# Performance work log

Hardware: AMD Instinct MI355X
Metric: run time of the kernel (lower is better)

## Reference

```python
import jax, jax.numpy as jnp
import numpy as np

NUM_FIELDS = 39
VOCAB_PER_FIELD = 1000
EMB = 64
HEADS = 2
LAYERS = 3
BATCH = 16384
FLAT = NUM_FIELDS * EMB  # 2496


def _mhsa(x, Wq, Wk, Wv, Wr):
    # x: [B, n, D]; no scaling (scaling=False in source)
    B, n, D = x.shape
    dh = D // HEADS
    q = (x @ Wq).reshape(B, n, HEADS, dh)
    k = (x @ Wk).reshape(B, n, HEADS, dh)
    v = (x @ Wv).reshape(B, n, HEADS, dh)
    scores = jnp.einsum('bihd,bjhd->bhij', q, k)
    attn = jax.nn.softmax(scores, axis=-1)
    out = jnp.einsum('bhij,bjhd->bihd', attn, v).reshape(B, n, D)
    out = out + x @ Wr  # residual projection (use_res=True)
    return jax.nn.relu(out)


def setup_inputs() -> dict:
    key = jax.random.key(0)
    ks = jax.random.split(key, 12)
    X = jax.random.randint(ks[0], (BATCH, NUM_FIELDS), 0, VOCAB_PER_FIELD, dtype=jnp.int64 if jax.config.jax_enable_x64 else jnp.int32)
    emb_table = jax.random.normal(ks[1], (NUM_FIELDS * VOCAB_PER_FIELD, EMB), jnp.float32) * 0.05
    WQ = jax.random.normal(ks[2], (LAYERS, EMB, EMB), jnp.float32) * 0.05
    WK = jax.random.normal(ks[3], (LAYERS, EMB, EMB), jnp.float32) * 0.05
    WV = jax.random.normal(ks[4], (LAYERS, EMB, EMB), jnp.float32) * 0.05
    WR = jax.random.normal(ks[5], (LAYERS, EMB, EMB), jnp.float32) * 0.05
    W1 = jax.random.normal(ks[6], (FLAT, 512), jnp.float32) * 0.02
    b1 = jnp.zeros((512,), jnp.float32)
    W2 = jax.random.normal(ks[7], (512, 256), jnp.float32) * 0.02
    b2 = jnp.zeros((256,), jnp.float32)
    W3 = jax.random.normal(ks[8], (256, 1), jnp.float32) * 0.02
    b3 = jnp.zeros((1,), jnp.float32)
    Wlin = jax.random.normal(ks[9], (FLAT, 1), jnp.float32) * 0.02
    return {"X": X, "emb_table": emb_table, "WQ": WQ, "WK": WK, "WV": WV,
            "WR": WR, "W1": W1, "b1": b1, "W2": W2, "b2": b2, "W3": W3,
            "b3": b3, "Wlin": Wlin}


def reference(X, emb_table, WQ, WK, WV, WR, W1, b1, W2, b2, W3, b3, Wlin):
    offsets = jnp.arange(NUM_FIELDS, dtype=X.dtype) * VOCAB_PER_FIELD
    embed_x = emb_table[X + offsets[None, :]]  # [B, n, D]
    att = embed_x
    for i in range(LAYERS):
        att = _mhsa(att, WQ[i], WK[i], WV[i], WR[i])
    B = att.shape[0]
    att_output = jax.nn.relu(att.reshape(B, FLAT) @ Wlin)  # [B,1]
    # MLP: relu follows every Dense, including final 1-unit layer; dropout inactive
    h = embed_x.reshape(B, FLAT)
    h = jax.nn.relu(h @ W1 + b1)
    h = jax.nn.relu(h @ W2 + b2)
    dnn_output = jax.nn.relu(h @ W3 + b3)  # [B,1]
    return jax.nn.sigmoid(att_output + dnn_output)
```

## Files before the change

### kernel.cpp

```cpp
#include <hip/hip_runtime.h>
#include <hip/hip_bf16.h>


#define NF     39
#define EMB    64
#define NLAYER 3
#define VOCAB  1000
#define FLAT   2496
#define H1     512
#define H2     256

typedef __attribute__((ext_vector_type(8))) short  short8;
typedef __attribute__((ext_vector_type(4))) float  floatx4;

__device__ __forceinline__ short8 ld8s(const unsigned short* p) {
    return *(const short8*)p;
}
__device__ __forceinline__ float b2f(unsigned short h) {
    union { unsigned u; float f; } x; x.u = ((unsigned)h) << 16; return x.f;
}
__device__ __forceinline__ unsigned short f2b(float f) {
    union { float f; unsigned u; } x; x.f = f;
    unsigned u = x.u;
    return (unsigned short)((u + 0x7fffu + ((u >> 16) & 1u)) >> 16);
}
__device__ __forceinline__ unsigned cvt_pk(float a, float b) {
#if defined(__gfx950__)
    unsigned r;
    asm("v_cvt_pk_bf16_f32 %0, %1, %2" : "=v"(r) : "v"(a), "v"(b));
    return r;
#else
    return (unsigned)f2b(a) | ((unsigned)f2b(b) << 16);
#endif
}

__global__ void attw_t(const float* __restrict__ WQ, const float* __restrict__ WK,
                       const float* __restrict__ WV, const float* __restrict__ WR,
                       unsigned short* __restrict__ wqt, unsigned short* __restrict__ wkt,
                       unsigned short* __restrict__ wvt, unsigned short* __restrict__ wrt)
{
    int idx = blockIdx.x * 256 + threadIdx.x;
    if (idx >= 4 * 3 * 4096) return;
    int mat = idx / 12288;
    int rem = idx % 12288;
    int l   = rem / 4096;
    int ok  = rem % 4096;
    int o = ok >> 6, k = ok & 63;
    const float*    src = (mat == 0) ? WQ : (mat == 1) ? WK : (mat == 2) ? WV : WR;
    unsigned short* dst = (mat == 0) ? wqt : (mat == 1) ? wkt : (mat == 2) ? wvt : wrt;
    dst[l * 4096 + o * 64 + k] = f2b(src[l * 4096 + k * 64 + o]);
}

__global__ void w1pack(const float* __restrict__ W1, unsigned short* __restrict__ w1p)
{
    int t = blockIdx.x * 256 + threadIdx.x;
    int lane = t & 63, grp = t >> 6;
    int ot = grp / 78, kk = grp % 78;
    int q = lane >> 4, n = ot * 16 + (lane & 15);
    int kb = kk * 32 + q * 8;
    unsigned short* dst = w1p + grp * 512 + lane * 8;
    #pragma unroll
    for (int j = 0; j < 8; ++j)
        dst[j] = f2b(W1[(kb + j) * 512 + n]);
}

__global__ void w2pack(const float* __restrict__ W2, unsigned short* __restrict__ w2p)
{
    int t = blockIdx.x * 256 + threadIdx.x;
    int lane = t & 63, grp = t >> 6;
    int ot = grp / 16, kk = grp % 16;
    int q = lane >> 4, n = ot * 16 + (lane & 15);
    int kb = kk * 32 + q * 8;
    unsigned short* dst = w2p + grp * 512 + lane * 8;
    #pragma unroll
    for (int j = 0; j < 8; ++j)
        dst[j] = f2b(W2[(kb + j) * 256 + n]);
}

__global__ void __launch_bounds__(256) attn_kernel(
    const int* __restrict__ X,
    const float* __restrict__ embf,
    const unsigned short* __restrict__ wqt,
    const unsigned short* __restrict__ wkt,
    const unsigned short* __restrict__ wvt,
    const unsigned short* __restrict__ wrt,
    const float* __restrict__ wlinf,
    float* __restrict__ att_out)
{
    __shared__ unsigned short xs[2][48 * 72];
    __shared__ unsigned short arena[4][4736];
    __shared__ float red[4];

    const int tid  = threadIdx.x;
    const int wid  = tid >> 6;
    const int lane = tid & 63;
    const int sl   = wid >> 1;
    const int h    = wid & 1;
    const int quad = lane >> 4;
    const int l16  = lane & 15;
    const int samp = blockIdx.x * 2 + sl;

    unsigned short* xss = xs[sl];
    unsigned short* qs  = arena[wid];
    unsigned short* ks  = qs + 1920;
    unsigned short* Ps  = qs;
    unsigned short* vt  = qs + 3456;

    {
        const int tq = lane >> 4;
        const int cp = (lane & 15) * 2;
        const int col = h * 32 + cp;
        const int* xrow = X + samp * NF;
        #pragma unroll
        for (int t0 = 0; t0 < 48; t0 += 4) {
            int t = t0 + tq;
            unsigned pk = 0;
            if (t < NF) {
                int row = xrow[t] + t * VOCAB;
                const float2 v = *(const float2*)&embf[row * EMB + col];
                pk = cvt_pk(v.x, v.y);
            }
            *(unsigned*)&xss[t * 72 + col] = pk;
        }
    }
    __syncthreads();

    for (int layer = 0; layer < NLAYER; ++layer) {
        const unsigned short* wq  = wqt + layer * 4096;
        const unsigned short* wk  = wkt + layer * 4096;
        const unsigned short* wvp = wvt + layer * 4096;
        const unsigned short* wr  = wrt + layer * 4096;

        #pragma unroll
        for (int mat = 0; mat < 2; ++mat) {
            const unsigned short* wt = mat ? wk : wq;
            unsigned short* dst = mat ? ks : qs;
            #pragma unroll
            for (int mt = 0; mt < 3; ++mt) {
                #pragma unroll
                for (int nt = 0; nt < 2; ++nt) {
                    floatx4 c = {0.f, 0.f, 0.f, 0.f};
                    #pragma unroll
                    for (int kk = 0; kk < 2; ++kk) {
                        short8 a = ld8s(&xss[(mt * 16 + l16) * 72 + kk * 32 + quad * 8]);
                        short8 b = ld8s(&wt[(h * 32 + nt * 16 + l16) * 64 + kk * 32 + quad * 8]);
                        c = __builtin_amdgcn_mfma_f32_16x16x32_bf16(a, b, c, 0, 0, 0);
                    }
                    unsigned plo = cvt_pk(c[0], c[1]);
                    unsigned phi = cvt_pk(c[2], c[3]);
                    int base = (mt * 16 + quad * 4) * 40 + nt * 16 + l16;
                    dst[base]       = (unsigned short)plo;
                    dst[base + 40]  = (unsigned short)(plo >> 16);
                    dst[base + 80]  = (unsigned short)phi;
                    dst[base + 120] = (unsigned short)(phi >> 16);
                }
            }
        }

        floatx4 ST[3][3];
        #pragma unroll
        for (int jt = 0; jt < 3; ++jt) {
            short8 a = ld8s(&ks[(jt * 16 + l16) * 40 + quad * 8]);
            #pragma unroll
            for (int it = 0; it < 3; ++it) {
                short8 b = ld8s(&qs[(it * 16 + l16) * 40 + quad * 8]);
                floatx4 z = {0.f, 0.f, 0.f, 0.f};
                ST[jt][it] = __builtin_amdgcn_mfma_f32_16x16x32_bf16(a, b, z, 0, 0, 0);
            }
        }

        #pragma unroll
        for (int it = 0; it < 3; ++it) {
            float p[3][4];
            float sum = 0.f;
            #pragma unroll
            for (int jt = 0; jt < 3; ++jt)
                #pragma unroll
                for (int r = 0; r < 4; ++r) {
                    int j = jt * 16 + quad * 4 + r;
                    float e = (j < NF) ? __expf(ST[jt][it][r]) : 0.f;
                    p[jt][r] = e;
                    sum += e;
                }
            sum += __shfl_xor(sum, 16, 64);
            sum += __shfl_xor(sum, 32, 64);
            float inv = 1.0f / sum;
            #pragma unroll
            for (int jt = 0; jt < 3; ++jt) {
                uint2 w;
                w.x = cvt_pk(p[jt][0] * inv, p[jt][1] * inv);
                w.y = cvt_pk(p[jt][2] * inv, p[jt][3] * inv);
                *(uint2*)&Ps[(it * 16 + l16) * 72 + jt * 16 + quad * 4] = w;
            }
            uint2 z2; z2.x = 0; z2.y = 0;
            *(uint2*)&Ps[(it * 16 + l16) * 72 + 48 + quad * 4] = z2;
        }

        unsigned sv[2][2];
        #pragma unroll
        for (int mt = 0; mt < 3; ++mt) {
            #pragma unroll
            for (int nt = 0; nt < 2; ++nt) {
                floatx4 c = {0.f, 0.f, 0.f, 0.f};
                #pragma unroll
                for (int kk = 0; kk < 2; ++kk) {
                    short8 a = ld8s(&xss[(mt * 16 + l16) * 72 + kk * 32 + quad * 8]);
                    short8 b = ld8s(&wvp[(h * 32 + nt * 16 + l16) * 64 + kk * 32 + quad * 8]);
                    c = __builtin_amdgcn_mfma_f32_16x16x32_bf16(a, b, c, 0, 0, 0);
                }
                unsigned lo = cvt_pk(c[0], c[1]);
                unsigned hi = cvt_pk(c[2], c[3]);
                if (mt < 2) {
                    uint2 w; w.x = lo; w.y = hi;
                    *(uint2*)&vt[(nt * 16 + l16) * 40 + mt * 16 + quad * 4] = w;
                } else {
                    sv[nt][0] = lo; sv[nt][1] = hi;
                }
            }
        }

        floatx4 O[3][2];
        #pragma unroll
        for (int mt = 0; mt < 3; ++mt) {
            #pragma unroll
            for (int nt = 0; nt < 2; ++nt) {
                floatx4 c = {0.f, 0.f, 0.f, 0.f};
                #pragma unroll
                for (int kk = 0; kk < 2; ++kk) {
                    short8 a = ld8s(&xss[(mt * 16 + l16) * 72 + kk * 32 + quad * 8]);
                    short8 b = ld8s(&wr[(h * 32 + nt * 16 + l16) * 64 + kk * 32 + quad * 8]);
                    c = __builtin_amdgcn_mfma_f32_16x16x32_bf16(a, b, c, 0, 0, 0);
                }
                O[mt][nt] = c;
            }
        }

        __syncthreads();

        {
            short8 a0 = ld8s(&Ps[(l16) * 72 + quad * 8]);
            short8 a1 = ld8s(&Ps[(16 + l16) * 72 + quad * 8]);
            short8 a2 = ld8s(&Ps[(32 + l16) * 72 + quad * 8]);
            #pragma unroll
            for (int nt = 0; nt < 2; ++nt) {
                short8 b = ld8s(&vt[(nt * 16 + l16) * 40 + quad * 8]);
                O[0][nt] = __builtin_amdgcn_mfma_f32_16x16x32_bf16(a0, b, O[0][nt], 0, 0, 0);
                O[1][nt] = __builtin_amdgcn_mfma_f32_16x16x32_bf16(a1, b, O[1][nt], 0, 0, 0);
                O[2][nt] = __builtin_amdgcn_mfma_f32_16x16x32_bf16(a2, b, O[2][nt], 0, 0, 0);
            }
        }
        #pragma unroll
        for (int nt = 0; nt < 2; ++nt) {
            uint2 w; w.x = sv[nt][0]; w.y = sv[nt][1];
            *(uint2*)&vt[(nt * 16 + l16) * 40 + quad * 4] = w;
            uint2 z; z.x = 0; z.y = 0;
            *(uint2*)&vt[(nt * 16 + l16) * 40 + 16 + quad * 4] = z;
        }
        {
            short8 a0 = ld8s(&Ps[(l16) * 72 + 32 + quad * 8]);
            short8 a1 = ld8s(&Ps[(16 + l16) * 72 + 32 + quad * 8]);
            short8 a2 = ld8s(&Ps[(32 + l16) * 72 + 32 + quad * 8]);
            #pragma unroll
            for (int nt = 0; nt < 2; ++nt) {
                short8 b = ld8s(&vt[(nt * 16 + l16) * 40 + quad * 8]);
                O[0][nt] = __builtin_amdgcn_mfma_f32_16x16x32_bf16(a0, b, O[0][nt], 0, 0, 0);
                O[1][nt] = __builtin_amdgcn_mfma_f32_16x16x32_bf16(a1, b, O[1][nt], 0, 0, 0);
                O[2][nt] = __builtin_amdgcn_mfma_f32_16x16x32_bf16(a2, b, O[2][nt], 0, 0, 0);
            }
        }

        #pragma unroll
        for (int mt = 0; mt < 3; ++mt)
            #pragma unroll
            for (int nt = 0; nt < 2; ++nt) {
                unsigned plo = cvt_pk(fmaxf(O[mt][nt][0], 0.f), fmaxf(O[mt][nt][1], 0.f));
                unsigned phi = cvt_pk(fmaxf(O[mt][nt][2], 0.f), fmaxf(O[mt][nt][3], 0.f));
                int base = (mt * 16 + quad * 4) * 72 + h * 32 + nt * 16 + l16;
                xss[base]       = (unsigned short)plo;
                xss[base + 72]  = (unsigned short)(plo >> 16);
                xss[base + 144] = (unsigned short)phi;
                xss[base + 216] = (unsigned short)(phi >> 16);
            }

        __syncthreads();
    }

    {
        float acc = 0.f;
        const int c = lane & 31, tp = lane >> 5;
        const int col = h * 32 + c;
        for (int t0 = 0; t0 < 40; t0 += 2) {
            int t = t0 + tp;
            if (t < NF)
                acc += b2f(xss[t * 72 + col]) * wlinf[t * EMB + col];
        }
        #pragma unroll
        for (int off = 1; off < 64; off <<= 1)
            acc += __shfl_xor(acc, off, 64);
        if (lane == 0) red[wid] = acc;
        __syncthreads();
        if (tid < 2) {
            float v2 = red[tid * 2] + red[tid * 2 + 1];
            att_out[blockIdx.x * 2 + tid] = fmaxf(v2, 0.f);
        }
    }
}

__global__ void __launch_bounds__(256) dnn_kernel(
    const int* __restrict__ X,
    const float* __restrict__ embf,
    const unsigned short* __restrict__ w1p,
    const float* __restrict__ b1v,
    const unsigned short* __restrict__ w2p,
    const float* __restrict__ b2v,
    const float* __restrict__ w3v,
    const float* __restrict__ b3v,
    const float* __restrict__ att_in,
    float* __restrict__ out)
{
    __shared__ unsigned short ea[2][32 * 72];
    __shared__ unsigned short h1s[32 * 520];
    unsigned short* h2s = h1s;

    const int tid  = threadIdx.x;
    const int wid  = tid >> 6, lane = tid & 63, quad = lane >> 4, l16 = lane & 15;
    const int S0   = blockIdx.x * 32;

    floatx4 C1[2][8];
    #pragma unroll
    for (int mt = 0; mt < 2; ++mt)
        #pragma unroll
        for (int nt = 0; nt < 8; ++nt)
            C1[mt][nt] = (floatx4){0.f, 0.f, 0.f, 0.f};

    const int gs = tid >> 3;
    const int gg = tid & 7;

    {
        int row = X[(S0 + gs) * NF + 0];
        const float4* src = (const float4*)&embf[row * EMB + gg * 8];
        float4 v0 = src[0], v1 = src[1];
        uint4 u;
        u.x = cvt_pk(v0.x, v0.y); u.y = cvt_pk(v0.z, v0.w);
        u.z = cvt_pk(v1.x, v1.y); u.w = cvt_pk(v1.z, v1.w);
        *(uint4*)&ea[0][gs * 72 + gg * 8] = u;
    }
    __syncthreads();

    for (int f = 0; f < NF; ++f) {
        if (f < NF - 1) {
            int row = X[(S0 + gs) * NF + f + 1] + (f + 1) * VOCAB;
            const float4* src = (const float4*)&embf[row * EMB + gg * 8];
            float4 v0 = src[0], v1 = src[1];
            uint4 u;
            u.x = cvt_pk(v0.x, v0.y); u.y = cvt_pk(v0.z, v0.w);
            u.z = cvt_pk(v1.x, v1.y); u.w = cvt_pk(v1.z, v1.w);
            *(uint4*)&ea[(f + 1) & 1][gs * 72 + gg * 8] = u;
        }
        const unsigned short* eac = ea[f & 1];
        short8 a[2][2];
        #pragma unroll
        for (int mt = 0; mt < 2; ++mt) {
            a[mt][0] = ld8s(&eac[(mt * 16 + l16) * 72 + quad * 8]);
            a[mt][1] = ld8s(&eac[(mt * 16 + l16) * 72 + 32 + quad * 8]);
        }
        #pragma unroll
        for (int nt = 0; nt < 8; ++nt) {
            const unsigned short* bp = w1p + (((wid * 8 + nt) * 78 + f * 2) * 64 + lane) * 8;
            short8 b0 = ld8s(bp);
            short8 b1 = ld8s(bp + 512);
            #pragma unroll
            for (int mt = 0; mt < 2; ++mt) {
                C1[mt][nt] = __builtin_amdgcn_mfma_f32_16x16x32_bf16(a[mt][0], b0, C1[mt][nt], 0, 0, 0);
                C1[mt][nt] = __builtin_amdgcn_mfma_f32_16x16x32_bf16(a[mt][1], b1, C1[mt][nt], 0, 0, 0);
            }
        }
        __syncthreads();
    }

    #pragma unroll
    for (int nt = 0; nt < 8; ++nt) {
        float bb = b1v[wid * 128 + nt * 16 + l16];
        #pragma unroll
        for (int mt = 0; mt < 2; ++mt) {
            #pragma unroll
            for (int r = 0; r < 4; ++r) {
                float v = fmaxf(C1[mt][nt][r] + bb, 0.f);
                h1s[(mt * 16 + quad * 4 + r) * 520 + wid * 128 + nt * 16 + l16] = f2b(v);
            }
        }
    }
    __syncthreads();

    floatx4 C2[2][4];
    #pragma unroll
    for (int mt = 0; mt < 2; ++mt)
        #pragma unroll
        for (int nt = 0; nt < 4; ++nt)
            C2[mt][nt] = (floatx4){0.f, 0.f, 0.f, 0.f};

    #pragma unroll 4
    for (int kk = 0; kk < 16; ++kk) {
        short8 a0 = ld8s(&h1s[(l16) * 520 + kk * 32 + quad * 8]);
        short8 a1 = ld8s(&h1s[(16 + l16) * 520 + kk * 32 + quad * 8]);
        #pragma unroll
        for (int nt = 0; nt < 4; ++nt) {
            short8 b = ld8s(w2p + (((wid * 4 + nt) * 16 + kk) * 64 + lane) * 8);
            C2[0][nt] = __builtin_amdgcn_mfma_f32_16x16x32_bf16(a0, b, C2[0][nt], 0, 0, 0);
            C2[1][nt] = __builtin_amdgcn_mfma_f32_16x16x32_bf16(a1, b, C2[1][nt], 0, 0, 0);
        }
    }
    __syncthreads();

    #pragma unroll
    for (int nt = 0; nt < 4; ++nt) {
        float bb = b2v[wid * 64 + nt * 16 + l16];
        #pragma unroll
        for (int mt = 0; mt < 2; ++mt)
            #pragma unroll
            for (int r = 0; r < 4; ++r)
                h2s[(mt * 16 + quad * 4 + r) * 264 + wid * 64 + nt * 16 + l16] =
                    f2b(fmaxf(C2[mt][nt][r] + bb, 0.f));
    }
    __syncthreads();

    {
        int s = tid >> 3, part = tid & 7;
        float acc = 0.f;
        #pragma unroll 8
        for (int j = 0; j < 32; ++j) {
            int jj = part * 32 + j;
            acc += b2f(h2s[s * 264 + jj]) * w3v[jj];
        }
        acc += __shfl_xor(acc, 1, 64);
        acc += __shfl_xor(acc, 2, 64);
        acc += __shfl_xor(acc, 4, 64);
        if (part == 0) {
            float dnn = fmaxf(acc + b3v[0], 0.f);
            float v = dnn + att_in[S0 + s];
            out[S0 + s] = 1.f / (1.f + __expf(-v));
        }
    }
}

extern "C" void kernel_launch(void* const* d_in, const int* in_sizes, int n_in,
                              void* d_out, int out_size, void* d_ws, size_t ws_size,
                              hipStream_t stream)
{
    (void)in_sizes; (void)n_in; (void)out_size; (void)ws_size;

    const int*   X    = (const int*)d_in[0];
    const float* emb  = (const float*)d_in[1];
    const float* WQ   = (const float*)d_in[2];
    const float* WK   = (const float*)d_in[3];
    const float* WV   = (const float*)d_in[4];
    const float* WR   = (const float*)d_in[5];
    const float* W1   = (const float*)d_in[6];
    const float* b1   = (const float*)d_in[7];
    const float* W2   = (const float*)d_in[8];
    const float* b2   = (const float*)d_in[9];
    const float* W3   = (const float*)d_in[10];
    const float* b3   = (const float*)d_in[11];
    const float* Wlin = (const float*)d_in[12];

    char* ws = (char*)d_ws;
    float*          att_logit = (float*)ws;
    unsigned short* wqt = (unsigned short*)(ws + 65536);
    unsigned short* wkt = wqt + 3 * 4096;
    unsigned short* wvt = wkt + 3 * 4096;
    unsigned short* wrt = wvt + 3 * 4096;
    unsigned short* w1p = wrt + 3 * 4096;
    unsigned short* w2p = w1p + 2496 * 512;

    attw_t<<<192, 256, 0, stream>>>(WQ, WK, WV, WR, wqt, wkt, wvt, wrt);
    w1pack<<<624, 256, 0, stream>>>(W1, w1p);
    w2pack<<<64, 256, 0, stream>>>(W2, w2p);
    attn_kernel<<<8192, 256, 0, stream>>>(X, emb, wqt, wkt, wvt, wrt, Wlin, att_logit);
    dnn_kernel<<<512, 256, 0, stream>>>(X, emb, w1p, b1, w2p, b2, W3, b3, att_logit,
                                        (float*)d_out);
}
```

Measured before the change: 418.8 us.

## Merge attention and DNN kernels into one heterogeneous-block launch

Combines the attention and MLP kernels into a single launch where every 17th block runs a 32-sample DNN tile and the rest run two-sample attention. The intent is to let the memory-bound DNN work overlap with the attention blocks on the GPU instead of running serially, and to remove the tail of the small 512-block DNN launch. A tiny combine kernel then applies the sigmoid. This costs a shared-memory footprint sized to the larger of the two roles, which may lower occupancy for the attention blocks, plus an extra launch and an extra workspace buffer.

```diff
diff --git a/kernel.cpp b/kernel.cpp
--- a/kernel.cpp
+++ b/kernel.cpp
@@ -77,7 +77,7 @@
         dst[j] = f2b(W2[(kb + j) * 256 + n]);
 }
 
-__global__ void __launch_bounds__(256) attn_kernel(
+__global__ void __launch_bounds__(256) fused_kernel(
     const int* __restrict__ X,
     const float* __restrict__ embf,
     const unsigned short* __restrict__ wqt,
@@ -85,362 +85,366 @@
     const unsigned short* __restrict__ wvt,
     const unsigned short* __restrict__ wrt,
     const float* __restrict__ wlinf,
-    float* __restrict__ att_out)
-{
-    __shared__ unsigned short xs[2][48 * 72];
-    __shared__ unsigned short arena[4][4736];
-    __shared__ float red[4];
-
-    const int tid  = threadIdx.x;
-    const int wid  = tid >> 6;
-    const int lane = tid & 63;
-    const int sl   = wid >> 1;
-    const int h    = wid & 1;
-    const int quad = lane >> 4;
-    const int l16  = lane & 15;
-    const int samp = blockIdx.x * 2 + sl;
-
-    unsigned short* xss = xs[sl];
-    unsigned short* qs  = arena[wid];
-    unsigned short* ks  = qs + 1920;
-    unsigned short* Ps  = qs;
-    unsigned short* vt  = qs + 3456;
-
-    {
-        const int tq = lane >> 4;
-        const int cp = (lane & 15) * 2;
-        const int col = h * 32 + cp;
-        const int* xrow = X + samp * NF;
-        #pragma unroll
-        for (int t0 = 0; t0 < 48; t0 += 4) {
-            int t = t0 + tq;
-            unsigned pk = 0;
-            if (t < NF) {
-                int row = xrow[t] + t * VOCAB;
-                const float2 v = *(const float2*)&embf[row * EMB + col];
-                pk = cvt_pk(v.x, v.y);
-            }
-            *(unsigned*)&xss[t * 72 + col] = pk;
-        }
-    }
-    __syncthreads();
-
-    for (int layer = 0; layer < NLAYER; ++layer) {
-        const unsigned short* wq  = wqt + layer * 4096;
-        const unsigned short* wk  = wkt + layer * 4096;
-        const unsigned short* wvp = wvt + layer * 4096;
-        const unsigned short* wr  = wrt + layer * 4096;
-
-        #pragma unroll
-        for (int mat = 0; mat < 2; ++mat) {
-            const unsigned short* wt = mat ? wk : wq;
-            unsigned short* dst = mat ? ks : qs;
-            #pragma unroll
-            for (int mt = 0; mt < 3; ++mt) {
-                #pragma unroll
-                for (int nt = 0; nt < 2; ++nt) {
-                    floatx4 c = {0.f, 0.f, 0.f, 0.f};
-                    #pragma unroll
-                    for (int kk = 0; kk < 2; ++kk) {
-                        short8 a = ld8s(&xss[(mt * 16 + l16) * 72 + kk * 32 + quad * 8]);
-                        short8 b = ld8s(&wt[(h * 32 + nt * 16 + l16) * 64 + kk * 32 + quad * 8]);
-                        c = __builtin_amdgcn_mfma_f32_16x16x32_bf16(a, b, c, 0, 0, 0);
-                    }
-                    unsigned plo = cvt_pk(c[0], c[1]);
-                    unsigned phi = cvt_pk(c[2], c[3]);
-                    int base = (mt * 16 + quad * 4) * 40 + nt * 16 + l16;
-                    dst[base]       = (unsigned short)plo;
-                    dst[base + 40]  = (unsigned short)(plo >> 16);
-                    dst[base + 80]  = (unsigned short)phi;
-                    dst[base + 120] = (unsigned short)(phi >> 16);
-                }
-            }
-        }
-
-        floatx4 ST[3][3];
-        #pragma unroll
-        for (int jt = 0; jt < 3; ++jt) {
-            short8 a = ld8s(&ks[(jt * 16 + l16) * 40 + quad * 8]);
-            #pragma unroll
-            for (int it = 0; it < 3; ++it) {
-                short8 b = ld8s(&qs[(it * 16 + l16) * 40 + quad * 8]);
-                floatx4 z = {0.f, 0.f, 0.f, 0.f};
-                ST[jt][it] = __builtin_amdgcn_mfma_f32_16x16x32_bf16(a, b, z, 0, 0, 0);
-            }
-        }
-
-        #pragma unroll
-        for (int it = 0; it < 3; ++it) {
-            float p[3][4];
-            float sum = 0.f;
-            #pragma unroll
-            for (int jt = 0; jt < 3; ++jt)
-                #pragma unroll
-                for (int r = 0; r < 4; ++r) {
-                    int j = jt * 16 + quad * 4 + r;
-                    float e = (j < NF) ? __expf(ST[jt][it][r]) : 0.f;
-                    p[jt][r] = e;
-                    sum += e;
-                }
-            sum += __shfl_xor(sum, 16, 64);
-            sum += __shfl_xor(sum, 32, 64);
-            float inv = 1.0f / sum;
-            #pragma unroll
-            for (int jt = 0; jt < 3; ++jt) {
-                uint2 w;
-                w.x = cvt_pk(p[jt][0] * inv, p[jt][1] * inv);
-                w.y = cvt_pk(p[jt][2] * inv, p[jt][3] * inv);
-                *(uint2*)&Ps[(it * 16 + l16) * 72 + jt * 16 + quad * 4] = w;
-            }
-            uint2 z2; z2.x = 0; z2.y = 0;
-            *(uint2*)&Ps[(it * 16 + l16) * 72 + 48 + quad * 4] = z2;
-        }
-
-        unsigned sv[2][2];
-        #pragma unroll
-        for (int mt = 0; mt < 3; ++mt) {
-            #pragma unroll
-            for (int nt = 0; nt < 2; ++nt) {
-                floatx4 c = {0.f, 0.f, 0.f, 0.f};
-                #pragma unroll
-                for (int kk = 0; kk < 2; ++kk) {
-                    short8 a = ld8s(&xss[(mt * 16 + l16) * 72 + kk * 32 + quad * 8]);
-                    short8 b = ld8s(&wvp[(h * 32 + nt * 16 + l16) * 64 + kk * 32 + quad * 8]);
-                    c = __builtin_amdgcn_mfma_f32_16x16x32_bf16(a, b, c, 0, 0, 0);
-                }
-                unsigned lo = cvt_pk(c[0], c[1]);
-                unsigned hi = cvt_pk(c[2], c[3]);
-                if (mt < 2) {
-                    uint2 w; w.x = lo; w.y = hi;
-                    *(uint2*)&vt[(nt * 16 + l16) * 40 + mt * 16 + quad * 4] = w;
-                } else {
-                    sv[nt][0] = lo; sv[nt][1] = hi;
-                }
-            }
-        }
-
-        floatx4 O[3][2];
-        #pragma unroll
-        for (int mt = 0; mt < 3; ++mt) {
-            #pragma unroll
-            for (int nt = 0; nt < 2; ++nt) {
-                floatx4 c = {0.f, 0.f, 0.f, 0.f};
-                #pragma unroll
-                for (int kk = 0; kk < 2; ++kk) {
-                    short8 a = ld8s(&xss[(mt * 16 + l16) * 72 + kk * 32 + quad * 8]);
-                    short8 b = ld8s(&wr[(h * 32 + nt * 16 + l16) * 64 + kk * 32 + quad * 8]);
-                    c = __builtin_amdgcn_mfma_f32_16x16x32_bf16(a, b, c, 0, 0, 0);
-                }
-                O[mt][nt] = c;
-            }
-        }
-
-        __syncthreads();
-
-        {
-            short8 a0 = ld8s(&Ps[(l16) * 72 + quad * 8]);
-            short8 a1 = ld8s(&Ps[(16 + l16) * 72 + quad * 8]);
-            short8 a2 = ld8s(&Ps[(32 + l16) * 72 + quad * 8]);
-            #pragma unroll
-            for (int nt = 0; nt < 2; ++nt) {
-                short8 b = ld8s(&vt[(nt * 16 + l16) * 40 + quad * 8]);
-                O[0][nt] = __builtin_amdgcn_mfma_f32_16x16x32_bf16(a0, b, O[0][nt], 0, 0, 0);
-                O[1][nt] = __builtin_amdgcn_mfma_f32_16x16x32_bf16(a1, b, O[1][nt], 0, 0, 0);
-                O[2][nt] = __builtin_amdgcn_mfma_f32_16x16x32_bf16(a2, b, O[2][nt], 0, 0, 0);
-            }
-        }
-        #pragma unroll
-        for (int nt = 0; nt < 2; ++nt) {
-            uint2 w; w.x = sv[nt][0]; w.y = sv[nt][1];
-            *(uint2*)&vt[(nt * 16 + l16) * 40 + quad * 4] = w;
-            uint2 z; z.x = 0; z.y = 0;
-            *(uint2*)&vt[(nt * 16 + l16) * 40 + 16 + quad * 4] = z;
-        }
-        {
-            short8 a0 = ld8s(&Ps[(l16) * 72 + 32 + quad * 8]);
-            short8 a1 = ld8s(&Ps[(16 + l16) * 72 + 32 + quad * 8]);
-            short8 a2 = ld8s(&Ps[(32 + l16) * 72 + 32 + quad * 8]);
-            #pragma unroll
-            for (int nt = 0; nt < 2; ++nt) {
-                short8 b = ld8s(&vt[(nt * 16 + l16) * 40 + quad * 8]);
-                O[0][nt] = __builtin_amdgcn_mfma_f32_16x16x32_bf16(a0, b, O[0][nt], 0, 0, 0);
-                O[1][nt] = __builtin_amdgcn_mfma_f32_16x16x32_bf16(a1, b, O[1][nt], 0, 0, 0);
-                O[2][nt] = __builtin_amdgcn_mfma_f32_16x16x32_bf16(a2, b, O[2][nt], 0, 0, 0);
-            }
-        }
-
-        #pragma unroll
-        for (int mt = 0; mt < 3; ++mt)
-            #pragma unroll
-            for (int nt = 0; nt < 2; ++nt) {
-                unsigned plo = cvt_pk(fmaxf(O[mt][nt][0], 0.f), fmaxf(O[mt][nt][1], 0.f));
-                unsigned phi = cvt_pk(fmaxf(O[mt][nt][2], 0.f), fmaxf(O[mt][nt][3], 0.f));
-                int base = (mt * 16 + quad * 4) * 72 + h * 32 + nt * 16 + l16;
-                xss[base]       = (unsigned short)plo;
-                xss[base + 72]  = (unsigned short)(plo >> 16);
-                xss[base + 144] = (unsigned short)phi;
-                xss[base + 216] = (unsigned short)(phi >> 16);
-            }
-
-        __syncthreads();
-    }
-
-    {
-        float acc = 0.f;
-        const int c = lane & 31, tp = lane >> 5;
-        const int col = h * 32 + c;
-        for (int t0 = 0; t0 < 40; t0 += 2) {
-            int t = t0 + tp;
-            if (t < NF)
-                acc += b2f(xss[t * 72 + col]) * wlinf[t * EMB + col];
-        }
-        #pragma unroll
-        for (int off = 1; off < 64; off <<= 1)
-            acc += __shfl_xor(acc, off, 64);
-        if (lane == 0) red[wid] = acc;
-        __syncthreads();
-        if (tid < 2) {
-            float v2 = red[tid * 2] + red[tid * 2 + 1];
-            att_out[blockIdx.x * 2 + tid] = fmaxf(v2, 0.f);
-        }
-    }
-}
-
-__global__ void __launch_bounds__(256) dnn_kernel(
-    const int* __restrict__ X,
-    const float* __restrict__ embf,
     const unsigned short* __restrict__ w1p,
     const float* __restrict__ b1v,
     const unsigned short* __restrict__ w2p,
     const float* __restrict__ b2v,
     const float* __restrict__ w3v,
     const float* __restrict__ b3v,
-    const float* __restrict__ att_in,
-    float* __restrict__ out)
-{
-    __shared__ unsigned short ea[2][32 * 72];
-    __shared__ unsigned short h1s[32 * 520];
-    unsigned short* h2s = h1s;
+    float* __restrict__ att_out,
+    float* __restrict__ dnn_out)
+{
+    __shared__ unsigned short smem[26112];
 
     const int tid  = threadIdx.x;
-    const int wid  = tid >> 6, lane = tid & 63, quad = lane >> 4, l16 = lane & 15;
-    const int S0   = blockIdx.x * 32;
-
-    floatx4 C1[2][8];
-    #pragma unroll
-    for (int mt = 0; mt < 2; ++mt)
+    const int wid  = tid >> 6;
+    const int lane = tid & 63;
+    const int quad = lane >> 4;
+    const int l16  = lane & 15;
+    const unsigned b = blockIdx.x;
+
+    if (b % 17 != 16) {
+        const int ablk = (int)(b - (b + 1) / 17);
+        const int sl   = wid >> 1;
+        const int h    = wid & 1;
+        const int samp = ablk * 2 + sl;
+
+        unsigned short* xss = smem + sl * 3456;
+        unsigned short* qs  = smem + 6912 + wid * 4736;
+        unsigned short* ks  = qs + 1920;
+        unsigned short* Ps  = qs;
+        unsigned short* vt  = qs + 3456;
+        float* red = (float*)(smem + 25856);
+
+        {
+            const int tq = lane >> 4;
+            const int cp = (lane & 15) * 2;
+            const int col = h * 32 + cp;
+            const int* xrow = X + samp * NF;
+            #pragma unroll
+            for (int t0 = 0; t0 < 48; t0 += 4) {
+                int t = t0 + tq;
+                unsigned pk = 0;
+                if (t < NF) {
+                    int row = xrow[t] + t * VOCAB;
+                    const float2 v = *(const float2*)&embf[row * EMB + col];
+                    pk = cvt_pk(v.x, v.y);
+                }
+                *(unsigned*)&xss[t * 72 + col] = pk;
+            }
+        }
+        __syncthreads();
+
+        for (int layer = 0; layer < NLAYER; ++layer) {
+            const unsigned short* wq  = wqt + layer * 4096;
+            const unsigned short* wk  = wkt + layer * 4096;
+            const unsigned short* wvp = wvt + layer * 4096;
+            const unsigned short* wr  = wrt + layer * 4096;
+
+            #pragma unroll
+            for (int mat = 0; mat < 2; ++mat) {
+                const unsigned short* wt = mat ? wk : wq;
+                unsigned short* dst = mat ? ks : qs;
+                #pragma unroll
+                for (int mt = 0; mt < 3; ++mt) {
+                    #pragma unroll
+                    for (int nt = 0; nt < 2; ++nt) {
+                        floatx4 c = {0.f, 0.f, 0.f, 0.f};
+                        #pragma unroll
+                        for (int kk = 0; kk < 2; ++kk) {
+                            short8 a = ld8s(&xss[(mt * 16 + l16) * 72 + kk * 32 + quad * 8]);
+                            short8 bb = ld8s(&wt[(h * 32 + nt * 16 + l16) * 64 + kk * 32 + quad * 8]);
+                            c = __builtin_amdgcn_mfma_f32_16x16x32_bf16(a, bb, c, 0, 0, 0);
+                        }
+                        unsigned plo = cvt_pk(c[0], c[1]);
+                        unsigned phi = cvt_pk(c[2], c[3]);
+                        int base = (mt * 16 + quad * 4) * 40 + nt * 16 + l16;
+                        dst[base]       = (unsigned short)plo;
+                        dst[base + 40]  = (unsigned short)(plo >> 16);
+                        dst[base + 80]  = (unsigned short)phi;
+                        dst[base + 120] = (unsigned short)(phi >> 16);
+                    }
+                }
+            }
+
+            floatx4 ST[3][3];
+            #pragma unroll
+            for (int jt = 0; jt < 3; ++jt) {
+                short8 a = ld8s(&ks[(jt * 16 + l16) * 40 + quad * 8]);
+                #pragma unroll
+                for (int it = 0; it < 3; ++it) {
+                    short8 bb = ld8s(&qs[(it * 16 + l16) * 40 + quad * 8]);
+                    floatx4 z = {0.f, 0.f, 0.f, 0.f};
+                    ST[jt][it] = __builtin_amdgcn_mfma_f32_16x16x32_bf16(a, bb, z, 0, 0, 0);
+                }
+            }
+
+            #pragma unroll
+            for (int it = 0; it < 3; ++it) {
+                float p[3][4];
+                float sum = 0.f;
+                #pragma unroll
+                for (int jt = 0; jt < 3; ++jt)
+                    #pragma unroll
+                    for (int r = 0; r < 4; ++r) {
+                        int j = jt * 16 + quad * 4 + r;
+                        float e = (j < NF) ? __expf(ST[jt][it][r]) : 0.f;
+                        p[jt][r] = e;
+                        sum += e;
+                    }
+                sum += __shfl_xor(sum, 16, 64);
+                sum += __shfl_xor(sum, 32, 64);
+                float inv = 1.0f / sum;
+                #pragma unroll
+                for (int jt = 0; jt < 3; ++jt) {
+                    uint2 w;
+                    w.x = cvt_pk(p[jt][0] * inv, p[jt][1] * inv);
+                    w.y = cvt_pk(p[jt][2] * inv, p[jt][3] * inv);
+                    *(uint2*)&Ps[(it * 16 + l16) * 72 + jt * 16 + quad * 4] = w;
+                }
+                uint2 z2; z2.x = 0; z2.y = 0;
+                *(uint2*)&Ps[(it * 16 + l16) * 72 + 48 + quad * 4] = z2;
+            }
+
+            unsigned sv[2][2];
+            #pragma unroll
+            for (int mt = 0; mt < 3; ++mt) {
+                #pragma unroll
+                for (int nt = 0; nt < 2; ++nt) {
+                    floatx4 c = {0.f, 0.f, 0.f, 0.f};
+                    #pragma unroll
+                    for (int kk = 0; kk < 2; ++kk) {
+                        short8 a = ld8s(&xss[(mt * 16 + l16) * 72 + kk * 32 + quad * 8]);
+                        short8 bb = ld8s(&wvp[(h * 32 + nt * 16 + l16) * 64 + kk * 32 + quad * 8]);
+                        c = __builtin_amdgcn_mfma_f32_16x16x32_bf16(a, bb, c, 0, 0, 0);
+                    }
+                    unsigned lo = cvt_pk(c[0], c[1]);
+                    unsigned hi = cvt_pk(c[2], c[3]);
+                    if (mt < 2) {
+                        uint2 w; w.x = lo; w.y = hi;
+                        *(uint2*)&vt[(nt * 16 + l16) * 40 + mt * 16 + quad * 4] = w;
+                    } else {
+                        sv[nt][0] = lo; sv[nt][1] = hi;
+                    }
+                }
+            }
+
+            floatx4 O[3][2];
+            #pragma unroll
+            for (int mt = 0; mt < 3; ++mt) {
+                #pragma unroll
+                for (int nt = 0; nt < 2; ++nt) {
+                    floatx4 c = {0.f, 0.f, 0.f, 0.f};
+                    #pragma unroll
+                    for (int kk = 0; kk < 2; ++kk) {
+                        short8 a = ld8s(&xss[(mt * 16 + l16) * 72 + kk * 32 + quad * 8]);
+                        short8 bb = ld8s(&wr[(h * 32 + nt * 16 + l16) * 64 + kk * 32 + quad * 8]);
+                        c = __builtin_amdgcn_mfma_f32_16x16x32_bf16(a, bb, c, 0, 0, 0);
+                    }
+                    O[mt][nt] = c;
+                }
+            }
+
+            __syncthreads();
+
+            {
+                short8 a0 = ld8s(&Ps[(l16) * 72 + quad * 8]);
+                short8 a1 = ld8s(&Ps[(16 + l16) * 72 + quad * 8]);
+                short8 a2 = ld8s(&Ps[(32 + l16) * 72 + quad * 8]);
+                #pragma unroll
+                for (int nt = 0; nt < 2; ++nt) {
+                    short8 bb = ld8s(&vt[(nt * 16 + l16) * 40 + quad * 8]);
+                    O[0][nt] = __builtin_amdgcn_mfma_f32_16x16x32_bf16(a0, bb, O[0][nt], 0, 0, 0);
+                    O[1][nt] = __builtin_amdgcn_mfma_f32_16x16x32_bf16(a1, bb, O[1][nt], 0, 0, 0);
+                    O[2][nt] = __builtin_amdgcn_mfma_f32_16x16x32_bf16(a2, bb, O[2][nt], 0, 0, 0);
+                }
+            }
+            #pragma unroll
+            for (int nt = 0; nt < 2; ++nt) {
+                uint2 w; w.x = sv[nt][0]; w.y = sv[nt][1];
+                *(uint2*)&vt[(nt * 16 + l16) * 40 + quad * 4] = w;
+                uint2 z; z.x = 0; z.y = 0;
+                *(uint2*)&vt[(nt * 16 + l16) * 40 + 16 + quad * 4] = z;
+            }
+            {
+                short8 a0 = ld8s(&Ps[(l16) * 72 + 32 + quad * 8]);
+                short8 a1 = ld8s(&Ps[(16 + l16) * 72 + 32 + quad * 8]);
+                short8 a2 = ld8s(&Ps[(32 + l16) * 72 + 32 + quad * 8]);
+                #pragma unroll
+                for (int nt = 0; nt < 2; ++nt) {
+                    short8 bb = ld8s(&vt[(nt * 16 + l16) * 40 + quad * 8]);
+                    O[0][nt] = __builtin_amdgcn_mfma_f32_16x16x32_bf16(a0, bb, O[0][nt], 0, 0, 0);
+                    O[1][nt] = __builtin_amdgcn_mfma_f32_16x16x32_bf16(a1, bb, O[1][nt], 0, 0, 0);
+                    O[2][nt] = __builtin_amdgcn_mfma_f32_16x16x32_bf16(a2, bb, O[2][nt], 0, 0, 0);
+                }
+            }
+
+            #pragma unroll
+            for (int mt = 0; mt < 3; ++mt)
+                #pragma unroll
+                for (int nt = 0; nt < 2; ++nt) {
+                    unsigned plo = cvt_pk(fmaxf(O[mt][nt][0], 0.f), fmaxf(O[mt][nt][1], 0.f));
+                    unsigned phi = cvt_pk(fmaxf(O[mt][nt][2], 0.f), fmaxf(O[mt][nt][3], 0.f));
+                    int base = (mt * 16 + quad * 4) * 72 + h * 32 + nt * 16 + l16;
+                    xss[base]       = (unsigned short)plo;
+                    xss[base + 72]  = (unsigned short)(plo >> 16);
+                    xss[base + 144] = (unsigned short)phi;
+                    xss[base + 216] = (unsigned short)(phi >> 16);
+                }
+
+            __syncthreads();
+        }
+
+        {
+            float acc = 0.f;
+            const int c = lane & 31, tp = lane >> 5;
+            const int col = h * 32 + c;
+            for (int t0 = 0; t0 < 40; t0 += 2) {
+                int t = t0 + tp;
+                if (t < NF)
+                    acc += b2f(xss[t * 72 + col]) * wlinf[t * EMB + col];
+            }
+            #pragma unroll
+            for (int off = 1; off < 64; off <<= 1)
+                acc += __shfl_xor(acc, off, 64);
+            if (lane == 0) red[wid] = acc;
+            __syncthreads();
+            if (tid < 2) {
+                float v2 = red[tid * 2] + red[tid * 2 + 1];
+                att_out[ablk * 2 + tid] = fmaxf(v2, 0.f);
+            }
+        }
+    } else {
+        const int S0 = (int)(b / 17) * 32;
+
+        unsigned short* ea0 = smem;
+        unsigned short* ea1 = smem + 2304;
+        unsigned short* h1s = smem + 4608;
+        unsigned short* h2s = h1s;
+
+        floatx4 C1[2][8];
         #pragma unroll
-        for (int nt = 0; nt < 8; ++nt)
-            C1[mt][nt] = (floatx4){0.f, 0.f, 0.f, 0.f};
-
-    const int gs = tid >> 3;
-    const int gg = tid & 7;
-
-    {
-        int row = X[(S0 + gs) * NF + 0];
-        const float4* src = (const float4*)&embf[row * EMB + gg * 8];
-        float4 v0 = src[0], v1 = src[1];
-        uint4 u;
-        u.x = cvt_pk(v0.x, v0.y); u.y = cvt_pk(v0.z, v0.w);
-        u.z = cvt_pk(v1.x, v1.y); u.w = cvt_pk(v1.z, v1.w);
-        *(uint4*)&ea[0][gs * 72 + gg * 8] = u;
-    }
-    __syncthreads();
-
-    for (int f = 0; f < NF; ++f) {
-        if (f < NF - 1) {
-            int row = X[(S0 + gs) * NF + f + 1] + (f + 1) * VOCAB;
+        for (int mt = 0; mt < 2; ++mt)
+            #pragma unroll
+            for (int nt = 0; nt < 8; ++nt)
+                C1[mt][nt] = (floatx4){0.f, 0.f, 0.f, 0.f};
+
+        const int gs = tid >> 3;
+        const int gg = tid & 7;
+
+        {
+            int row = X[(S0 + gs) * NF + 0];
             const float4* src = (const float4*)&embf[row * EMB + gg * 8];
             float4 v0 = src[0], v1 = src[1];
             uint4 u;
             u.x = cvt_pk(v0.x, v0.y); u.y = cvt_pk(v0.z, v0.w);
             u.z = cvt_pk(v1.x, v1.y); u.w = cvt_pk(v1.z, v1.w);
-            *(uint4*)&ea[(f + 1) & 1][gs * 72 + gg * 8] = u;
-        }
-        const unsigned short* eac = ea[f & 1];
-        short8 a[2][2];
-        #pragma unroll
-        for (int mt = 0; mt < 2; ++mt) {
-            a[mt][0] = ld8s(&eac[(mt * 16 + l16) * 72 + quad * 8]);
-            a[mt][1] = ld8s(&eac[(mt * 16 + l16) * 72 + 32 + quad * 8]);
-        }
+            *(uint4*)&ea0[gs * 72 + gg * 8] = u;
+        }
+        __syncthreads();
+
+        for (int f = 0; f < NF; ++f) {
+            unsigned short* enext = ((f + 1) & 1) ? ea1 : ea0;
+            if (f < NF - 1) {
+                int row = X[(S0 + gs) * NF + f + 1] + (f + 1) * VOCAB;
+                const float4* src = (const float4*)&embf[row * EMB + gg * 8];
+                float4 v0 = src[0], v1 = src[1];
+                uint4 u;
+                u.x = cvt_pk(v0.x, v0.y); u.y = cvt_pk(v0.z, v0.w);
+                u.z = cvt_pk(v1.x, v1.y); u.w = cvt_pk(v1.z, v1.w);
+                *(uint4*)&enext[gs * 72 + gg * 8] = u;
+            }
+            const unsigned short* eac = (f & 1) ? ea1 : ea0;
+            short8 a[2][2];
+            #pragma unroll
+            for (int mt = 0; mt < 2; ++mt) {
+                a[mt][0] = ld8s(&eac[(mt * 16 + l16) * 72 + quad * 8]);
+                a[mt][1] = ld8s(&eac[(mt * 16 + l16) * 72 + 32 + quad * 8]);
+            }
+            #pragma unroll
+            for (int nt = 0; nt < 8; ++nt) {
+                const unsigned short* bp = w1p + (((wid * 8 + nt) * 78 + f * 2) * 64 + lane) * 8;
+                short8 b0 = ld8s(bp);
+                short8 b1 = ld8s(bp + 512);
+                #pragma unroll
+                for (int mt = 0; mt < 2; ++mt) {
+                    C1[mt][nt] = __builtin_amdgcn_mfma_f32_16x16x32_bf16(a[mt][0], b0, C1[mt][nt], 0, 0, 0);
+                    C1[mt][nt] = __builtin_amdgcn_mfma_f32_16x16x32_bf16(a[mt][1], b1, C1[mt][nt], 0, 0, 0);
+                }
+            }
+            __syncthreads();
+        }
+
         #pragma unroll
         for (int nt = 0; nt < 8; ++nt) {
-            const unsigned short* bp = w1p + (((wid * 8 + nt) * 78 + f * 2) * 64 + lane) * 8;
-            short8 b0 = ld8s(bp);
-            short8 b1 = ld8s(bp + 512);
+            float bb = b1v[wid * 128 + nt * 16 + l16];
             #pragma unroll
             for (int mt = 0; mt < 2; ++mt) {
-                C1[mt][nt] = __builtin_amdgcn_mfma_f32_16x16x32_bf16(a[mt][0], b0, C1[mt][nt], 0, 0, 0);
-                C1[mt][nt] = __builtin_amdgcn_mfma_f32_16x16x32_bf16(a[mt][1], b1, C1[mt][nt], 0, 0, 0);
+                #pragma unroll
+                for (int r = 0; r < 4; ++r) {
+                    float v = fmaxf(C1[mt][nt][r] + bb, 0.f);
+                    h1s[(mt * 16 + quad * 4 + r) * 520 + wid * 128 + nt * 16 + l16] = f2b(v);
+                }
             }
         }
         __syncthreads();
-    }
-
-    #pragma unroll
-    for (int nt = 0; nt < 8; ++nt) {
-        float bb = b1v[wid * 128 + nt * 16 + l16];
+
+        floatx4 C2[2][4];
         #pragma unroll
-        for (int mt = 0; mt < 2; ++mt) {
-            #pragma unroll
-            for (int r = 0; r < 4; ++r) {
-                float v = fmaxf(C1[mt][nt][r] + bb, 0.f);
-                h1s[(mt * 16 + quad * 4 + r) * 520 + wid * 128 + nt * 16 + l16] = f2b(v);
-            }
-        }
-    }
-    __syncthreads();
-
-    floatx4 C2[2][4];
-    #pragma unroll
-    for (int mt = 0; mt < 2; ++mt)
-        #pragma unroll
-        for (int nt = 0; nt < 4; ++nt)
-            C2[mt][nt] = (floatx4){0.f, 0.f, 0.f, 0.f};
-
-    #pragma unroll 4
-    for (int kk = 0; kk < 16; ++kk) {
-        short8 a0 = ld8s(&h1s[(l16) * 520 + kk * 32 + quad * 8]);
-        short8 a1 = ld8s(&h1s[(16 + l16) * 520 + kk * 32 + quad * 8]);
+        for (int mt = 0; mt < 2; ++mt)
+            #pragma unroll
+            for (int nt = 0; nt < 4; ++nt)
+                C2[mt][nt] = (floatx4){0.f, 0.f, 0.f, 0.f};
+
+        #pragma unroll 4
+        for (int kk = 0; kk < 16; ++kk) {
+            short8 a0 = ld8s(&h1s[(l16) * 520 + kk * 32 + quad * 8]);
+            short8 a1 = ld8s(&h1s[(16 + l16) * 520 + kk * 32 + quad * 8]);
+            #pragma unroll
+            for (int nt = 0; nt < 4; ++nt) {
+                short8 bb = ld8s(w2p + (((wid * 4 + nt) * 16 + kk) * 64 + lane) * 8);
+                C2[0][nt] = __builtin_amdgcn_mfma_f32_16x16x32_bf16(a0, bb, C2[0][nt], 0, 0, 0);
+                C2[1][nt] = __builtin_amdgcn_mfma_f32_16x16x32_bf16(a1, bb, C2[1][nt], 0, 0, 0);
+            }
+        }
+        __syncthreads();
+
         #pragma unroll
         for (int nt = 0; nt < 4; ++nt) {
-            short8 b = ld8s(w2p + (((wid * 4 + nt) * 16 + kk) * 64 + lane) * 8);
-            C2[0][nt] = __builtin_amdgcn_mfma_f32_16x16x32_bf16(a0, b, C2[0][nt], 0, 0, 0);
-            C2[1][nt] = __builtin_amdgcn_mfma_f32_16x16x32_bf16(a1, b, C2[1][nt], 0, 0, 0);
+            float bb = b2v[wid * 64 + nt * 16 + l16];
+            #pragma unroll
+            for (int mt = 0; mt < 2; ++mt)
+                #pragma unroll
+                for (int r = 0; r < 4; ++r)
+                    h2s[(mt * 16 + quad * 4 + r) * 264 + wid * 64 + nt * 16 + l16] =
+                        f2b(fmaxf(C2[mt][nt][r] + bb, 0.f));
+        }
+        __syncthreads();
+
+        {
+            int s = tid >> 3, part = tid & 7;
+            float acc = 0.f;
+            #pragma unroll 8
+            for (int j = 0; j < 32; ++j) {
+                int jj = part * 32 + j;
+                acc += b2f(h2s[s * 264 + jj]) * w3v[jj];
+            }
+            acc += __shfl_xor(acc, 1, 64);
+            acc += __shfl_xor(acc, 2, 64);
+            acc += __shfl_xor(acc, 4, 64);
+            if (part == 0)
+                dnn_out[S0 + s] = fmaxf(acc + b3v[0], 0.f);
         }
     }
-    __syncthreads();
-
-    #pragma unroll
-    for (int nt = 0; nt < 4; ++nt) {
-        float bb = b2v[wid * 64 + nt * 16 + l16];
-        #pragma unroll
-        for (int mt = 0; mt < 2; ++mt)
-            #pragma unroll
-            for (int r = 0; r < 4; ++r)
-                h2s[(mt * 16 + quad * 4 + r) * 264 + wid * 64 + nt * 16 + l16] =
-                    f2b(fmaxf(C2[mt][nt][r] + bb, 0.f));
-    }
-    __syncthreads();
-
-    {
-        int s = tid >> 3, part = tid & 7;
-        float acc = 0.f;
-        #pragma unroll 8
-        for (int j = 0; j < 32; ++j) {
-            int jj = part * 32 + j;
-            acc += b2f(h2s[s * 264 + jj]) * w3v[jj];
-        }
-        acc += __shfl_xor(acc, 1, 64);
-        acc += __shfl_xor(acc, 2, 64);
-        acc += __shfl_xor(acc, 4, 64);
-        if (part == 0) {
-            float dnn = fmaxf(acc + b3v[0], 0.f);
-            float v = dnn + att_in[S0 + s];
-            out[S0 + s] = 1.f / (1.f + __expf(-v));
-        }
-    }
+}
+
+__global__ void combine_kernel(const float* __restrict__ att,
+                               const float* __restrict__ dnnl,
+                               float* __restrict__ out)
+{
+    int i = blockIdx.x * 256 + threadIdx.x;
+    float v = att[i] + dnnl[i];
+    out[i] = 1.f / (1.f + __expf(-v));
 }
 
 extern "C" void kernel_launch(void* const* d_in, const int* in_sizes, int n_in,
@@ -465,7 +469,8 @@
 
     char* ws = (char*)d_ws;
     float*          att_logit = (float*)ws;
-    unsigned short* wqt = (unsigned short*)(ws + 65536);
+    float*          dnn_logit = (float*)(ws + 65536);
+    unsigned short* wqt = (unsigned short*)(ws + 131072);
     unsigned short* wkt = wqt + 3 * 4096;
     unsigned short* wvt = wkt + 3 * 4096;
     unsigned short* wrt = wvt + 3 * 4096;
@@ -475,7 +480,8 @@
     attw_t<<<192, 256, 0, stream>>>(WQ, WK, WV, WR, wqt, wkt, wvt, wrt);
     w1pack<<<624, 256, 0, stream>>>(W1, w1p);
     w2pack<<<64, 256, 0, stream>>>(W2, w2p);
-    attn_kernel<<<8192, 256, 0, stream>>>(X, emb, wqt, wkt, wvt, wrt, Wlin, att_logit);
-    dnn_kernel<<<512, 256, 0, stream>>>(X, emb, w1p, b1, w2p, b2, W3, b3, att_logit,
-                                        (float*)d_out);
-}
+    fused_kernel<<<8704, 256, 0, stream>>>(X, emb, wqt, wkt, wvt, wrt, Wlin,
+                                           w1p, b1, w2p, b2, W3, b3,
+                                           att_logit, dnn_logit);
+    combine_kernel<<<64, 256, 0, stream>>>(att_logit, dnn_logit, (float*)d_out);
+}
```

After: 489.9 us. 17.0% more time.
